# Performance work log

Measured on AMD Instinct MI355X. Metric: run time of the kernel, lower is better.

The kernel has to match this reference:

```python
import jax, jax.numpy as jnp
import numpy as np

N = 4096       # nodes
NFEAT = 256    # feature dim
NCLASS = 16
E = 65536      # edges = N * avg_degree(16)
NLAYER = 4
ALPHA = 0.5    # blancealpha (non-trainable)
LAMBDA_1 = 1.0
LAMBDA_2 = 1.0
EPS = 1e-12    # F.normalize eps


def setup_inputs() -> dict:
    key = jax.random.key(0)
    ks = jax.random.split(key, 9)
    feat = jax.random.normal(ks[0], (N, NFEAT), dtype=jnp.float32)
    z0 = jax.random.uniform(ks[1], (N, NFEAT), dtype=jnp.float32)       # torch.rand init of z
    w1 = jax.random.uniform(ks[2], (N, N), dtype=jnp.float32)           # uniform_(0,1)
    EA = jax.random.uniform(ks[3], (N, N), dtype=jnp.float32)           # uniform_(0,1)
    w2_w = jax.random.normal(ks[4], (2 * NFEAT, NCLASS), dtype=jnp.float32) * 0.05
    w2_b = jnp.zeros((NCLASS,), dtype=jnp.float32)
    edge_i = jax.random.randint(ks[5], (E,), 0, N, dtype=jnp.int32)
    edge_j = jax.random.randint(ks[6], (E,), 0, N, dtype=jnp.int32)
    edge_val = jax.random.uniform(ks[7], (E,), dtype=jnp.float32)
    # dense adjacency from the sparse edge list (coalesce -> duplicate indices sum)
    adj = jnp.zeros((N, N), dtype=jnp.float32).at[edge_i, edge_j].add(edge_val)
    # w22 = ones with zeros at edge positions (as in __init__)
    w22 = jnp.ones((N, N), dtype=jnp.float32).at[edge_i, edge_j].set(0.0)
    return dict(feat=feat, z0=z0, w1=w1, EA=EA, w2_w=w2_w, w2_b=w2_b,
                adj=adj, w22=w22, edge_val=edge_val, edge_i=edge_i, edge_j=edge_j)


def reference(feat, z0, w1, EA, w2_w, w2_b, adj, w22, edge_val, edge_i, edge_j):
    n = feat.shape[0]
    y = feat                      # y starts as feat
    z = z0                        # torch.rand init, passed in for determinism
    EP = jnp.ones((n, n), dtype=feat.dtype)
    masked_EA = ALPHA * EA * w22  # constant across layers
    for _ in range(NLAYER):
        # dropout is identity in eval mode (training=False)
        A = adj * EP + masked_EA            # [n, n]
        yyT = y @ y.T                       # [n, n] (reused; same values as the two torch.mm calls)
        temp = EP.T @ y + A @ y - yyT @ y   # [n, nfeat]
        temp = jax.nn.sigmoid(w1 @ temp)
        y_n = (LAMBDA_2 / 2) * temp + feat
        z_n = z - A @ z                     # (I - A) @ z
        # ans(z, adj): edgewise ||z_i - z_j|| * adj_val scattered to dense
        P = jnp.linalg.norm(z[edge_i] - z[edge_j], axis=1) * edge_val   # [E]
        M = jnp.zeros((n, n), dtype=z.dtype).at[edge_i, edge_j].add(P)
        EP = (LAMBDA_2 * (yyT - masked_EA) - LAMBDA_1 * 0.5 * M) / LAMBDA_2
        y, z = y_n, z_n
    # F.normalize(p=2, dim=1)
    y = y / jnp.maximum(jnp.linalg.norm(y, axis=1, keepdims=True), EPS)
    z = z / jnp.maximum(jnp.linalg.norm(z, axis=1, keepdims=True), EPS)
    p = jnp.concatenate([z, y], axis=1)     # [n, 2*nfeat]
    logits = p @ w2_w + w2_b
    return jax.nn.log_softmax(logits, axis=1)
```

## Files before the change

### kernel.cpp

```cpp
#include <hip/hip_runtime.h>

#define Nn 4096
#define Ff 256
#define NCLS 16
#define Ne 65536
#define TSZ 262144
#define NF (Nn*Ff)
#define NNx (Nn*Nn)
#define KS 8

typedef unsigned short u16;
typedef unsigned int u32;
typedef __attribute__((ext_vector_type(8))) short short8;
typedef __attribute__((ext_vector_type(4))) float float4v;

__device__ __forceinline__ float bfh(u16 u){ return __uint_as_float(((u32)u)<<16); }
__device__ __forceinline__ u16 f2bf(float f){
    u32 u = __float_as_uint(f);
    return (u16)((u + 0x7FFFu + ((u>>16)&1u)) >> 16);
}
__device__ __forceinline__ void gload16(const u16* g, u16* l){
    __builtin_amdgcn_global_load_lds(
        (const __attribute__((address_space(1))) u32*)(const void*)g,
        (__attribute__((address_space(3))) u32*)(void*)l, 16, 0, 0);
}

__device__ float g_yA[NF], g_yB[NF], g_zA[NF], g_zB[NF], g_t1[NF], g_T1[NF];
__device__ float g_Gp[16*Ff*Ff], g_col[Ff], g_P[Ne], g_cc[Ne], g_hV[TSZ];
__device__ float g_pb[(size_t)3*KS*NF];
__device__ u32 g_hK[TSZ], g_slot[Ne];
__device__ int g_cntI[Nn], g_cntJ[Nn], g_rpI[Nn+1], g_rpJ[Nn+1], g_fI[Nn], g_fJ[Nn];
__device__ int g_lI[Ne], g_lJ[Ne];
__device__ __align__(16) u16 g_w1h[NNx], g_w1l[NNx];
__device__ __align__(16) u16 g_meh[NNx], g_mel[NNx];
__device__ __align__(16) u16 g_mth[NNx], g_mtl[NNx];
__device__ __align__(16) u16 g_x0h[NF], g_x0l[NF], g_x1h[NF], g_x1l[NF];
__device__ __align__(16) u16 g_zt0h[NF], g_zt0l[NF], g_zt1h[NF], g_zt1l[NF];
__device__ __align__(16) u16 g_yr0h[NF], g_yr0l[NF], g_yr1h[NF], g_yr1l[NF];
__device__ __align__(16) u16 g_tth[NF], g_ttl[NF];
__device__ __align__(16) u16 g_gth[Ff*Ff], g_gtl[Ff*Ff];

__global__ __launch_bounds__(256) void k_zero(float* p, int n){
    int i = blockIdx.x*256 + threadIdx.x;
    if (i < n) p[i] = 0.f;
}
__global__ __launch_bounds__(256) void k_zeroi(int* p, int n){
    int i = blockIdx.x*256 + threadIdx.x;
    if (i < n) p[i] = 0;
}
__global__ __launch_bounds__(256) void k_fillc(float* p, float v, int n){
    int i = blockIdx.x*256 + threadIdx.x;
    if (i < n) p[i] = v;
}
__global__ __launch_bounds__(256) void k_hkeys_clear(u32* K){
    int i = blockIdx.x*256 + threadIdx.x;
    if (i < TSZ) K[i] = 0xFFFFFFFFu;
}
__global__ __launch_bounds__(256) void k_hsetup(u32* K, u32* slot, const int* ei, const int* ej){
    int e = blockIdx.x*256 + threadIdx.x;
    if (e >= Ne) return;
    u32 key = ((u32)ei[e] << 12) | (u32)ej[e];
    u32 h = (key * 2654435761u) & (TSZ-1);
    for (;;){
        u32 old = atomicCAS(&K[h], 0xFFFFFFFFu, key);
        if (old == 0xFFFFFFFFu || old == key){ slot[e] = h; break; }
        h = (h+1) & (TSZ-1);
    }
}

__global__ __launch_bounds__(256) void k_count(int* cntI, int* cntJ, const int* ei, const int* ej){
    int e = blockIdx.x*256 + threadIdx.x;
    if (e < Ne){ atomicAdd(&cntI[ei[e]], 1); atomicAdd(&cntJ[ej[e]], 1); }
}
// ... 48 lines not shown
    __syncthreads();
    for (int q = 0; q < 16; ++q){
        int r = q*4 + rr;
        float v = T[c][r];
        size_t o = (size_t)(c0+r)*Nn + r0 + c;
        u16 h = f2bf(v); mth[o] = h; mtl[o] = f2bf(v - bfh(h));
    }
}
__global__ __launch_bounds__(256) void k_splitXT(u16* hi, u16* lo, const float* X){
    __shared__ float T[64][65];
    int r0 = blockIdx.y*64, c0 = blockIdx.x*64;
    int c = threadIdx.x & 63, rr = threadIdx.x >> 6;
    for (int q = 0; q < 16; ++q){
        int r = q*4 + rr;
        T[r][c] = X[(size_t)(r0+r)*Ff + c0 + c];
    }
    __syncthreads();
    for (int q = 0; q < 16; ++q){
        int r = q*4 + rr;
        float v = T[c][r];
        size_t o = (size_t)(c0+r)*Nn + r0 + c;
        u16 h = f2bf(v); hi[o] = h; lo[o] = f2bf(v - bfh(h));
    }
}
__global__ __launch_bounds__(256) void k_splitGT(u16* hi, u16* lo, const float* Gp){
    __shared__ float T[64][65];
    int r0 = blockIdx.y*64, c0 = blockIdx.x*64;
    int c = threadIdx.x & 63, rr = threadIdx.x >> 6;
    for (int q = 0; q < 16; ++q){
        int r = q*4 + rr;
        float v = 0.f;
        #pragma unroll
        for (int z = 0; z < 16; ++z) v += Gp[z*(Ff*Ff) + (r0+r)*Ff + c0 + c];
        T[r][c] = v;
    }
    __syncthreads();
    for (int q = 0; q < 16; ++q){
        int r = q*4 + rr;
        float v = T[c][r];
        int o = (c0+r)*Ff + r0 + c;
        u16 h = f2bf(v); hi[o] = h; lo[o] = f2bf(v - bfh(h));
    }
}

__device__ __forceinline__ void mm_tile(
    const u16* __restrict__ Ahp, const u16* __restrict__ Alp,
    const u16* __restrict__ Bhp, const u16* __restrict__ Blp,
    size_t sA, size_t sB, int i0, int j0, int k0,
    u16* LAh, u16* LAl, u16* LBh, u16* LBl,
    float4v* acc, int lane, int w)
{
    const int g1 = w*64 + lane;
    const int g2 = g1 + 256;
    const int r1 = g1>>3, p1 = g1&7, r2 = g2>>3, p2 = g2&7;
    const size_t a1 = (size_t)(i0+r1)*sA + (size_t)(k0 + ((p1 ^ (r1&7))<<3));
    const size_t a2 = (size_t)(i0+r2)*sA + (size_t)(k0 + ((p2 ^ (r2&7))<<3));
    const size_t b1 = (size_t)(j0+r1)*sB + (size_t)(k0 + ((p1 ^ (r1&7))<<3));
    const size_t b2 = (size_t)(j0+r2)*sB + (size_t)(k0 + ((p2 ^ (r2&7))<<3));
    __syncthreads();
    gload16(Ahp + a1, LAh + g1*8);
    gload16(Ahp + a2, LAh + g2*8);
    gload16(Alp + a1, LAl + g1*8);
    gload16(Alp + a2, LAl + g2*8);
    gload16(Bhp + b1, LBh + g1*8);
    gload16(Bhp + b2, LBh + g2*8);
    gload16(Blp + b1, LBl + g1*8);
// ... 38 lines not shown
        for (int r = 0; r < 4; ++r){
            int grow = i0 + w*16 + (lane>>4)*4 + r;
            int gcol = j0 + c*16 + (lane&15);
            size_t idx = (size_t)grow*Ff + gcol;
            float v = acc[c][r];
            if constexpr (V == 3) out[idx] = aux1[idx] - v;
            if constexpr (V == 4) out[idx] = aux1[gcol] - v;
            if constexpr (V == 5) out[idx] = v;
        }
}

__global__ __launch_bounds__(256) void k_gram_mm(float* __restrict__ Gp,
        const u16* __restrict__ Ahp, const u16* __restrict__ Alp,
        const u16* __restrict__ Bhp, const u16* __restrict__ Blp){
    __shared__ u16 LAh[4096], LAl[4096], LBh[4096], LBl[4096];
    const int tid = threadIdx.x, lane = tid & 63, w = tid >> 6;
    const int j0 = blockIdx.x*64, i0 = blockIdx.y*64, kb = blockIdx.z*256;
    float4v acc[4];
    #pragma unroll
    for (int c = 0; c < 4; ++c) acc[c] = (float4v){0.f,0.f,0.f,0.f};
    for (int kt = 0; kt < 4; ++kt)
        mm_tile(Ahp, Alp, Bhp, Blp, (size_t)Nn, (size_t)Nn, i0, j0, kb + kt*64, LAh, LAl, LBh, LBl, acc, lane, w);
    float* op = Gp + (size_t)blockIdx.z*(Ff*Ff);
    #pragma unroll
    for (int c = 0; c < 4; ++c)
        #pragma unroll
        for (int r = 0; r < 4; ++r){
            int grow = i0 + w*16 + (lane>>4)*4 + r;
            int gcol = j0 + c*16 + (lane&15);
            op[grow*Ff + gcol] = acc[c][r];
        }
}

__global__ __launch_bounds__(512) void k_mmB(float* __restrict__ pb,
        const u16* __restrict__ A0h, const u16* __restrict__ A0l,
        const u16* __restrict__ B0h, const u16* __restrict__ B0l,
        const u16* __restrict__ A1h, const u16* __restrict__ A1l,
        const u16* __restrict__ B1h, const u16* __restrict__ B1l,
        const u16* __restrict__ A2h, const u16* __restrict__ A2l,
        const u16* __restrict__ B2h, const u16* __restrict__ B2l){
    __shared__ u16 LAh[4096], LAl[4096], LBh[16384], LBl[16384];
    const int tid = threadIdx.x, lane = tid & 63, w = tid >> 6;
    const int z = blockIdx.x, i0 = blockIdx.y*64, bat = blockIdx.z;
    const u16 *Ah, *Al, *Bh, *Bl;
    if (bat == 0){ Ah = A0h; Al = A0l; Bh = B0h; Bl = B0l; }
    else if (bat == 1){ Ah = A1h; Al = A1l; Bh = B1h; Bl = B1l; }
    else { Ah = A2h; Al = A2l; Bh = B2h; Bl = B2l; }
    const int wr = w >> 2, wc = w & 3;
    float4v acc[2][4];
    #pragma unroll
    for (int m = 0; m < 2; ++m)
        #pragma unroll
        for (int n = 0; n < 4; ++n) acc[m][n] = (float4v){0.f,0.f,0.f,0.f};

    const int ra = tid >> 3, pa = tid & 7;
    const size_t aoff = (size_t)(i0+ra)*Nn + (size_t)((pa ^ (ra&7))<<3);

    for (int kt = 0; kt < 8; ++kt){
        const int k0 = z*512 + kt*64;
        __syncthreads();
        gload16(Ah + aoff + k0, LAh + tid*8);
        gload16(Al + aoff + k0, LAl + tid*8);
        #pragma unroll
        for (int it = 0; it < 4; ++it){
            int g = it*512 + tid;
            int r = g >> 3, p = g & 7;
            size_t b = (size_t)r*Nn + (size_t)(k0 + ((p ^ (r&7))<<3));
            gload16(Bh + b, LBh + g*8);
            gload16(Bl + b, LBl + g*8);
        }
        __syncthreads();
        #pragma unroll
        for (int kk = 0; kk < 2; ++kk){
            const int ch = kk*4 + (lane>>4);
            short8 ah0, ah1, al0, al1;
            {
                const int arow = wr*32 + (lane&15);
                const int ao = arow*64 + ((ch ^ (arow&7))<<3);
                ah0 = *(const short8*)(LAh + ao);
                al0 = *(const short8*)(LAl + ao);
            }
            {
                const int arow = wr*32 + 16 + (lane&15);
                const int ao = arow*64 + ((ch ^ (arow&7))<<3);
                ah1 = *(const short8*)(LAh + ao);
                al1 = *(const short8*)(LAl + ao);
            }
            #pragma unroll
            for (int n = 0; n < 4; ++n){
                const int bcol = wc*64 + n*16 + (lane&15);
                const int bo = bcol*64 + ((ch ^ (bcol&7))<<3);
                short8 bh = *(const short8*)(LBh + bo);
                short8 bl = *(const short8*)(LBl + bo);
                acc[0][n] = __builtin_amdgcn_mfma_f32_16x16x32_bf16(ah0, bh, acc[0][n], 0,0,0);
                acc[0][n] = __builtin_amdgcn_mfma_f32_16x16x32_bf16(ah0, bl, acc[0][n], 0,0,0);
                acc[0][n] = __builtin_amdgcn_mfma_f32_16x16x32_bf16(al0, bh, acc[0][n], 0,0,0);
                acc[1][n] = __builtin_amdgcn_mfma_f32_16x16x32_bf16(ah1, bh, acc[1][n], 0,0,0);
                acc[1][n] = __builtin_amdgcn_mfma_f32_16x16x32_bf16(ah1, bl, acc[1][n], 0,0,0);
                acc[1][n] = __builtin_amdgcn_mfma_f32_16x16x32_bf16(al1, bh, acc[1][n], 0,0,0);
            }
        }
    }
    float* op = pb + ((size_t)bat*KS + z)*NF;
    #pragma unroll
    for (int m = 0; m < 2; ++m)
        #pragma unroll
        for (int n = 0; n < 4; ++n)
            #pragma unroll
            for (int r = 0; r < 4; ++r){
                int row = i0 + wr*32 + m*16 + (lane>>4)*4 + r;
                int col = wc*64 + n*16 + (lane&15);
                op[(size_t)row*Ff + col] = acc[m][n][r];
            }
}

template<int HASM, int DOSPLIT>
__global__ __launch_bounds__(256) void k_redT1(float* __restrict__ t1, const float* __restrict__ pb,
        u16* __restrict__ th, u16* __restrict__ tl){
    __shared__ float T[64][65];
    const int c0 = blockIdx.x*64, r0 = blockIdx.y*64;
    const int c = threadIdx.x & 63, rr = threadIdx.x >> 6;
    for (int q = 0; q < 16; ++q){
        int row = q*4 + rr;
        size_t idx = (size_t)(r0+row)*Ff + c0 + c;
        float s = 0.f;
        #pragma unroll
        for (int p = 0; p < KS; ++p) s += pb[(size_t)p*NF + idx];
        if constexpr (HASM){
            #pragma unroll
            for (int p = 0; p < KS; ++p) s -= pb[((size_t)2*KS + p)*NF + idx];
        }
        float val = t1[idx] + s;
        t1[idx] = val;
        if constexpr (DOSPLIT) T[row][c] = val;
    }
    if constexpr (DOSPLIT){
        __syncthreads();
        for (int q = 0; q < 16; ++q){
            int r = q*4 + rr;
            float v = T[c][r];
            size_t o = (size_t)(c0+r)*Nn + r0 + c;
            u16 h = f2bf(v); th[o] = h; tl[o] = f2bf(v - bfh(h));
        }
    }
}

__global__ __launch_bounds__(256) void k_redY(float* __restrict__ yn, const float* __restrict__ pb,
        const float* __restrict__ feat, u16* __restrict__ rh, u16* __restrict__ rl,
        u16* __restrict__ th, u16* __restrict__ tl){
    __shared__ float T[64][65];
    const int c0 = blockIdx.x*64, r0 = blockIdx.y*64;
    const int c = threadIdx.x & 63, rr = threadIdx.x >> 6;
    for (int q = 0; q < 16; ++q){
        int row = q*4 + rr;
        size_t idx = (size_t)(r0+row)*Ff + c0 + c;
        float s = 0.f;
        #pragma unroll
        for (int p = 0; p < KS; ++p) s += pb[(size_t)p*NF + idx];
        float val = feat[idx] + 0.5f*(1.f/(1.f+expf(-s)));
        yn[idx] = val;
        u16 h = f2bf(val); rh[idx] = h; rl[idx] = f2bf(val - bfh(h));
        T[row][c] = val;
    }
    __syncthreads();
    for (int q = 0; q < 16; ++q){
        int r = q*4 + rr;
        float v = T[c][r];
        size_t o = (size_t)(c0+r)*Nn + r0 + c;
        u16 h = f2bf(v); th[o] = h; tl[o] = f2bf(v - bfh(h));
    }
}

__global__ __launch_bounds__(256) void k_csrTZ(float* __restrict__ t1, float* __restrict__ zn,
        const float* __restrict__ y, const float* __restrict__ z, const float* __restrict__ pb1,
        const float* __restrict__ cc, const float* __restrict__ P,
        const int* __restrict__ rpI, const int* __restrict__ lI, const int* __restrict__ ej,
        const int* __restrict__ rpJ, const int* __restrict__ lJ, const int* __restrict__ ei,
        int useM){
    const int r = blockIdx.x, f = threadIdx.x;
    float at = 0.f, az = 0.f;
    const int b0 = rpI[r], b1 = rpI[r+1];
    for (int p = b0; p < b1; ++p){
        int e = lI[p];
        float ce = cc[e];
        int j = ej[e];
        at += ce * y[(size_t)j*Ff + f];
        az += ce * z[(size_t)j*Ff + f];
    }
    if (useM){
        const int c0 = rpJ[r], c1 = rpJ[r+1];
        for (int p = c0; p < c1; ++p){
            int e = lJ[p];
            at -= 0.5f * P[e] * y[(size_t)ei[e]*Ff + f];
        }
    }
    size_t idx = (size_t)r*Ff + f;
    float dz = 0.f;
    #pragma unroll
    for (int p = 0; p < KS; ++p) dz += pb1[(size_t)p*NF + idx];
    t1[idx] += at;
    zn[idx] = z[idx] - dz - az;
}

__global__ __launch_bounds__(256) void k_colsum(float* col, const float* __restrict__ y){
    int j = threadIdx.x;
    int r0 = blockIdx.x*64;
    float s = 0.f;
    for (int i = 0; i < 64; ++i) s += y[(size_t)(r0+i)*Ff + j];
    atomicAdd(&col[j], s);
}

__global__ __launch_bounds__(256) void k_pacc(float* __restrict__ P, float* __restrict__ hV,
        const float* __restrict__ z, const int* __restrict__ ei, const int* __restrict__ ej,
        const float* __restrict__ ev, const u32* __restrict__ slot){
    int e = blockIdx.x*4 + (threadIdx.x >> 6);
    int lane = threadIdx.x & 63;
    int i = ei[e], j = ej[e];
    float s = 0.f;
    #pragma unroll
    for (int q = 0; q < 4; ++q){
        int f = lane + q*64;
        float d = z[(size_t)i*Ff + f] - z[(size_t)j*Ff + f];
        s += d*d;
    }
    #pragma unroll
    for (int o = 32; o; o >>= 1) s += __shfl_xor(s, o);
    if (lane == 0){
        float v = sqrtf(s) * ev[e];
        P[e] = v;
        atomicAdd(&hV[slot[e]], v);
    }
}
// ... 60 lines not shown
        for (int cc = 0; cc < NCLS; ++cc) se += expf(lg[cc]-m);
        ml[0] = m; ml[1] = logf(se);
    }
    __syncthreads();
    if (t < NCLS) out[(size_t)node*NCLS + t] = lg[t] - ml[0] - ml[1];
}

extern "C" void kernel_launch(void* const* d_in, const int* in_sizes, int n_in,
                              void* d_out, int out_size, void* d_ws, size_t ws_size,
                              hipStream_t stream){
    const float* feat = (const float*)d_in[0];
    const float* z0i  = (const float*)d_in[1];
    const float* w1p  = (const float*)d_in[2];
    const float* EAp  = (const float*)d_in[3];
    const float* w2w  = (const float*)d_in[4];
    const float* w2b  = (const float*)d_in[5];
    const float* w22p = (const float*)d_in[7];
    const float* evp  = (const float*)d_in[8];
    const int* ei   = (const int*)d_in[9];
    const int* ej   = (const int*)d_in[10];
    float* out = (float*)d_out;

    int ok = (n_in == 11) && (out_size == Nn*NCLS)
           && in_sizes[0]==NF && in_sizes[1]==NF && in_sizes[2]==NNx && in_sizes[3]==NNx
           && in_sizes[4]==2*Ff*NCLS && in_sizes[5]==NCLS && in_sizes[6]==NNx && in_sizes[7]==NNx
           && in_sizes[8]==Ne && in_sizes[9]==Ne && in_sizes[10]==Ne;
    if (!ok){
        k_fillc<<<(out_size+255)/256, 256, 0, stream>>>(out, -100.0f, out_size);
        return;
    }

    float *yA,*yB,*zA,*zB,*t1,*T1,*Gp,*col,*P,*cc,*hV,*pb; u32 *hK,*slot;
    int *cntI,*cntJ,*rpI,*rpJ,*fI,*fJ,*lI,*lJ;
    u16 *w1h,*w1l,*meh,*mel,*mth,*mtl,*gth,*gtl,*tth,*ttl;
    u16 *xh[2],*xl[2],*zth[2],*ztl[2],*yrh[2],*yrl[2];
    hipGetSymbolAddress((void**)&yA,  HIP_SYMBOL(g_yA));
    hipGetSymbolAddress((void**)&yB,  HIP_SYMBOL(g_yB));
    hipGetSymbolAddress((void**)&zA,  HIP_SYMBOL(g_zA));
    hipGetSymbolAddress((void**)&zB,  HIP_SYMBOL(g_zB));
    hipGetSymbolAddress((void**)&t1,  HIP_SYMBOL(g_t1));
    hipGetSymbolAddress((void**)&T1,  HIP_SYMBOL(g_T1));
    hipGetSymbolAddress((void**)&Gp,  HIP_SYMBOL(g_Gp));
    hipGetSymbolAddress((void**)&col, HIP_SYMBOL(g_col));
    hipGetSymbolAddress((void**)&P,   HIP_SYMBOL(g_P));
    hipGetSymbolAddress((void**)&cc,  HIP_SYMBOL(g_cc));
    hipGetSymbolAddress((void**)&hV,  HIP_SYMBOL(g_hV));
    hipGetSymbolAddress((void**)&pb,  HIP_SYMBOL(g_pb));
    hipGetSymbolAddress((void**)&hK,  HIP_SYMBOL(g_hK));
    hipGetSymbolAddress((void**)&slot,HIP_SYMBOL(g_slot));
    hipGetSymbolAddress((void**)&cntI,HIP_SYMBOL(g_cntI));
    hipGetSymbolAddress((void**)&cntJ,HIP_SYMBOL(g_cntJ));
    hipGetSymbolAddress((void**)&rpI, HIP_SYMBOL(g_rpI));
    hipGetSymbolAddress((void**)&rpJ, HIP_SYMBOL(g_rpJ));
    hipGetSymbolAddress((void**)&fI,  HIP_SYMBOL(g_fI));
    hipGetSymbolAddress((void**)&fJ,  HIP_SYMBOL(g_fJ));
    hipGetSymbolAddress((void**)&lI,  HIP_SYMBOL(g_lI));
    hipGetSymbolAddress((void**)&lJ,  HIP_SYMBOL(g_lJ));
    hipGetSymbolAddress((void**)&w1h, HIP_SYMBOL(g_w1h));
    hipGetSymbolAddress((void**)&w1l, HIP_SYMBOL(g_w1l));
    hipGetSymbolAddress((void**)&meh, HIP_SYMBOL(g_meh));
    hipGetSymbolAddress((void**)&mel, HIP_SYMBOL(g_mel));
    hipGetSymbolAddress((void**)&mth, HIP_SYMBOL(g_mth));
    hipGetSymbolAddress((void**)&mtl, HIP_SYMBOL(g_mtl));
    hipGetSymbolAddress((void**)&gth, HIP_SYMBOL(g_gth));
    hipGetSymbolAddress((void**)&gtl, HIP_SYMBOL(g_gtl));
    hipGetSymbolAddress((void**)&tth, HIP_SYMBOL(g_tth));
    hipGetSymbolAddress((void**)&ttl, HIP_SYMBOL(g_ttl));
    hipGetSymbolAddress((void**)&xh[0], HIP_SYMBOL(g_x0h));
    hipGetSymbolAddress((void**)&xl[0], HIP_SYMBOL(g_x0l));
    hipGetSymbolAddress((void**)&xh[1], HIP_SYMBOL(g_x1h));
    hipGetSymbolAddress((void**)&xl[1], HIP_SYMBOL(g_x1l));
    hipGetSymbolAddress((void**)&zth[0], HIP_SYMBOL(g_zt0h));
    hipGetSymbolAddress((void**)&ztl[0], HIP_SYMBOL(g_zt0l));
    hipGetSymbolAddress((void**)&zth[1], HIP_SYMBOL(g_zt1h));
    hipGetSymbolAddress((void**)&ztl[1], HIP_SYMBOL(g_zt1l));
    hipGetSymbolAddress((void**)&yrh[0], HIP_SYMBOL(g_yr0h));
    hipGetSymbolAddress((void**)&yrl[0], HIP_SYMBOL(g_yr0l));
    hipGetSymbolAddress((void**)&yrh[1], HIP_SYMBOL(g_yr1h));
    hipGetSymbolAddress((void**)&yrl[1], HIP_SYMBOL(g_yr1l));

    const dim3 gSmall(Ff/64, Nn/64);
    const dim3 gXT(Ff/64, Nn/64);
    const dim3 gME(Nn/64, Nn/64);
    const dim3 gGT(Ff/64, Ff/64);
    const dim3 gGram(4, 4, 16);
    const dim3 gRed(Ff/64, Nn/64);

    k_split4<<<NNx/4/256, 256, 0, stream>>>((ushort4*)w1h, (ushort4*)w1l, (const float4*)w1p, NNx/4);
    k_splitME2<<<gME, 256, 0, stream>>>(meh, mel, mth, mtl, EAp, w22p);
    k_split4<<<NF/4/256, 256, 0, stream>>>((ushort4*)yrh[0], (ushort4*)yrl[0], (const float4*)feat, NF/4);
    k_splitXT<<<gXT, 256, 0, stream>>>(xh[0], xl[0], feat);
    k_splitXT<<<gXT, 256, 0, stream>>>(zth[0], ztl[0], z0i);
    k_hkeys_clear<<<TSZ/256, 256, 0, stream>>>(hK);
    k_hsetup<<<Ne/256, 256, 0, stream>>>(hK, slot, ei, ej);
    k_zeroi<<<Nn/256, 256, 0, stream>>>(cntI, Nn);
    k_zeroi<<<Nn/256, 256, 0, stream>>>(cntJ, Nn);
    k_count<<<Ne/256, 256, 0, stream>>>(cntI, cntJ, ei, ej);
    k_scan<<<1, 1024, 0, stream>>>(cntI, rpI);
    k_scan<<<1, 1024, 0, stream>>>(cntJ, rpJ);
    k_zeroi<<<Nn/256, 256, 0, stream>>>(fI, Nn);
    k_zeroi<<<Nn/256, 256, 0, stream>>>(fJ, Nn);
    k_fillcsr<<<Ne/256, 256, 0, stream>>>(rpI, rpJ, fI, fJ, lI, lJ, ei, ej);

    const float* yv = feat;  const float* zv = z0i;
    for (int t = 1; t <= 4; ++t){
        int ri = (t-1) & 1, wi = t & 1;
        u16 *xhc = xh[ri], *xlc = xl[ri], *xhn = xh[wi], *xln = xl[wi];
        u16 *zthc = zth[ri], *ztlc = ztl[ri], *zthn = zth[wi], *ztln = ztl[wi];
        u16 *yrhc = yrh[ri], *yrlc = yrl[ri], *yrhn = yrh[wi], *yrln = yrl[wi];
        float* yn = (t & 1) ? yA : yB;
        float* zn = (t & 1) ? zA : zB;
        const float* ccv = (t == 1) ? evp : cc;

        k_gram_mm<<<gGram, 256, 0, stream>>>(Gp, xhc, xlc, xhc, xlc);
        k_splitGT<<<gGT, 256, 0, stream>>>(gth, gtl, Gp);
        if (t == 1){
            k_zero<<<1, 256, 0, stream>>>(col, Ff);
            k_colsum<<<64, 256, 0, stream>>>(col, yv);
            k_mm<4><<<gSmall, 256, 0, stream>>>(t1, yrhc, yrlc, gth, gtl, col);
        } else {
            k_mm<3><<<gSmall, 256, 0, stream>>>(t1, yrhc, yrlc, gth, gtl, T1);
        }
        {
            int nb = (t == 1) ? 2 : 3;
            dim3 gB(KS, Nn/64, nb);
            k_mmB<<<gB, 512, 0, stream>>>(pb,
                meh, mel, xhc, xlc,
                meh, mel, zthc, ztlc,
                mth, mtl, xhc, xlc);
        }
        k_csrTZ<<<Nn, 256, 0, stream>>>(t1, zn, yv, zv, pb + (size_t)KS*NF, ccv, P,
                                        rpI, lI, ej, rpJ, lJ, ei, (t >= 2) ? 1 : 0);
        if (t == 1) k_redT1<0,1><<<gRed, 256, 0, stream>>>(t1, pb, tth, ttl);
        else        k_redT1<1,1><<<gRed, 256, 0, stream>>>(t1, pb, tth, ttl);
        if (t < 4)
            k_splitXT<<<gXT, 256, 0, stream>>>(zthn, ztln, zn);
        {
            dim3 gB(KS, Nn/64, 1);
            k_mmB<<<gB, 512, 0, stream>>>(pb,
                w1h, w1l, tth, ttl,
                w1h, w1l, tth, ttl,
                w1h, w1l, tth, ttl);
        }
        k_redY<<<gRed, 256, 0, stream>>>(yn, pb, feat, yrhn, yrln, xhn, xln);
        if (t < 4){
            k_zero<<<TSZ/256, 256, 0, stream>>>(hV, TSZ);
            k_pacc<<<Ne/4, 256, 0, stream>>>(P, hV, zv, ei, ej, evp, slot);
            k_ep<<<Ne/4, 256, 0, stream>>>(cc, yv, ei, ej, evp, hV, slot);
            k_gram_mm<<<gGram, 256, 0, stream>>>(Gp, xhc, xlc, xhn, xln);
            k_splitGT<<<gGT, 256, 0, stream>>>(gth, gtl, Gp);
            k_mm<5><<<gSmall, 256, 0, stream>>>(T1, yrhc, yrlc, gth, gtl, nullptr);
        }
        yv = yn; zv = zn;
    }
    k_head<<<Nn, 256, 0, stream>>>(out, yv, zv, w2w, w2b);
}
```

Baseline: 1.479 ms.

## Double-buffer LDS in split-bf16 GEMM and retile to 128x128 blocks

The split-K bf16x3 GEMM kernel now stages the next 64-wide K slice into a second LDS buffer while computing on the current one, replacing the load-sync-compute-sync pattern. The block tile changes from 64 rows by all 256 columns to 128x128, with wave layout 4x2, and the grid is reshaped so blockIdx.x encodes column half and K split. The aim is to hide global-to-LDS latency and balance A and B tile loads. In exchange, LDS use per block doubles to 128KB, which limits occupancy. There is also no wait on the async global_load_lds before the barrier, so it relies on the barrier's implicit vmcnt behaviour.

Result: slower. 1.546 ms (+4.5%).

```diff
diff --git a/kernel.cpp b/kernel.cpp
--- a/kernel.cpp
+++ b/kernel.cpp
@@ -264,69 +264,74 @@
         const u16* __restrict__ B1h, const u16* __restrict__ B1l,
         const u16* __restrict__ A2h, const u16* __restrict__ A2l,
         const u16* __restrict__ B2h, const u16* __restrict__ B2l){
-    __shared__ u16 LAh[4096], LAl[4096], LBh[16384], LBl[16384];
+    __shared__ u16 LA[2][2][8192];
+    __shared__ u16 LB[2][2][8192];
     const int tid = threadIdx.x, lane = tid & 63, w = tid >> 6;
-    const int z = blockIdx.x, i0 = blockIdx.y*64, bat = blockIdx.z;
+    const int jb = blockIdx.x & 1, kp = blockIdx.x >> 1;
+    const int j0 = jb*128, i0 = blockIdx.y*128, bat = blockIdx.z;
+    const int kbase = kp*512;
     const u16 *Ah, *Al, *Bh, *Bl;
     if (bat == 0){ Ah = A0h; Al = A0l; Bh = B0h; Bl = B0l; }
     else if (bat == 1){ Ah = A1h; Al = A1l; Bh = B1h; Bl = B1l; }
     else { Ah = A2h; Al = A2l; Bh = B2h; Bl = B2l; }
-    const int wr = w >> 2, wc = w & 3;
+    const int wr = w >> 1, wc = w & 1;
     float4v acc[2][4];
     #pragma unroll
     for (int m = 0; m < 2; ++m)
         #pragma unroll
         for (int n = 0; n < 4; ++n) acc[m][n] = (float4v){0.f,0.f,0.f,0.f};
 
-    const int ra = tid >> 3, pa = tid & 7;
-    const size_t aoff = (size_t)(i0+ra)*Nn + (size_t)((pa ^ (ra&7))<<3);
-
+    const int srow = tid >> 3, sp = tid & 7;
+    const size_t aoff0 = (size_t)(i0 + srow)*Nn + (size_t)((sp ^ (srow&7))<<3);
+    const size_t aoff1 = aoff0 + (size_t)64*Nn;
+    const size_t boff0 = (size_t)(j0 + srow)*Nn + (size_t)((sp ^ (srow&7))<<3);
+    const size_t boff1 = boff0 + (size_t)64*Nn;
+    const int d0 = tid*8, d1 = tid*8 + 4096;
+
+#define STAGE(B, K0) { \
+    gload16(Ah + aoff0 + (K0), &LA[B][0][d0]); \
+    gload16(Ah + aoff1 + (K0), &LA[B][0][d1]); \
+    gload16(Al + aoff0 + (K0), &LA[B][1][d0]); \
+    gload16(Al + aoff1 + (K0), &LA[B][1][d1]); \
+    gload16(Bh + boff0 + (K0), &LB[B][0][d0]); \
+    gload16(Bh + boff1 + (K0), &LB[B][0][d1]); \
+    gload16(Bl + boff0 + (K0), &LB[B][1][d0]); \
+    gload16(Bl + boff1 + (K0), &LB[B][1][d1]); }
+
+#define COMPUTE(B) { \
+    _Pragma("unroll") \
+    for (int kk = 0; kk < 2; ++kk){ \
+        const int ch = kk*4 + (lane>>4); \
+        short8 ah0, al0, ah1, al1; \
+        { int ar = wr*32 + (lane&15); int ao = ar*64 + ((ch ^ (ar&7))<<3); \
+          ah0 = *(const short8*)&LA[B][0][ao]; al0 = *(const short8*)&LA[B][1][ao]; } \
+        { int ar = wr*32 + 16 + (lane&15); int ao = ar*64 + ((ch ^ (ar&7))<<3); \
+          ah1 = *(const short8*)&LA[B][0][ao]; al1 = *(const short8*)&LA[B][1][ao]; } \
+        _Pragma("unroll") \
+        for (int n = 0; n < 4; ++n){ \
+            int bc = wc*64 + n*16 + (lane&15); int bo = bc*64 + ((ch ^ (bc&7))<<3); \
+            short8 bh = *(const short8*)&LB[B][0][bo]; \
+            short8 bl = *(const short8*)&LB[B][1][bo]; \
+            acc[0][n] = __builtin_amdgcn_mfma_f32_16x16x32_bf16(ah0, bh, acc[0][n], 0,0,0); \
+            acc[0][n] = __builtin_amdgcn_mfma_f32_16x16x32_bf16(ah0, bl, acc[0][n], 0,0,0); \
+            acc[0][n] = __builtin_amdgcn_mfma_f32_16x16x32_bf16(al0, bh, acc[0][n], 0,0,0); \
+            acc[1][n] = __builtin_amdgcn_mfma_f32_16x16x32_bf16(ah1, bh, acc[1][n], 0,0,0); \
+            acc[1][n] = __builtin_amdgcn_mfma_f32_16x16x32_bf16(ah1, bl, acc[1][n], 0,0,0); \
+            acc[1][n] = __builtin_amdgcn_mfma_f32_16x16x32_bf16(al1, bh, acc[1][n], 0,0,0); \
+        } \
+    } }
+
+    STAGE(0, kbase)
+    __syncthreads();
     for (int kt = 0; kt < 8; ++kt){
-        const int k0 = z*512 + kt*64;
+        if (kt < 7) STAGE((kt+1)&1, kbase + (kt+1)*64)
+        COMPUTE(kt&1)
         __syncthreads();
-        gload16(Ah + aoff + k0, LAh + tid*8);
-        gload16(Al + aoff + k0, LAl + tid*8);
-        #pragma unroll
-        for (int it = 0; it < 4; ++it){
-            int g = it*512 + tid;
-            int r = g >> 3, p = g & 7;
-            size_t b = (size_t)r*Nn + (size_t)(k0 + ((p ^ (r&7))<<3));
-            gload16(Bh + b, LBh + g*8);
-            gload16(Bl + b, LBl + g*8);
-        }
-        __syncthreads();
-        #pragma unroll
-        for (int kk = 0; kk < 2; ++kk){
-            const int ch = kk*4 + (lane>>4);
-            short8 ah0, ah1, al0, al1;
-            {
-                const int arow = wr*32 + (lane&15);
-                const int ao = arow*64 + ((ch ^ (arow&7))<<3);
-                ah0 = *(const short8*)(LAh + ao);
-                al0 = *(const short8*)(LAl + ao);
-            }
-            {
-                const int arow = wr*32 + 16 + (lane&15);
-                const int ao = arow*64 + ((ch ^ (arow&7))<<3);
-                ah1 = *(const short8*)(LAh + ao);
-                al1 = *(const short8*)(LAl + ao);
-            }
-            #pragma unroll
-            for (int n = 0; n < 4; ++n){
-                const int bcol = wc*64 + n*16 + (lane&15);
-                const int bo = bcol*64 + ((ch ^ (bcol&7))<<3);
-                short8 bh = *(const short8*)(LBh + bo);
-                short8 bl = *(const short8*)(LBl + bo);
-                acc[0][n] = __builtin_amdgcn_mfma_f32_16x16x32_bf16(ah0, bh, acc[0][n], 0,0,0);
-                acc[0][n] = __builtin_amdgcn_mfma_f32_16x16x32_bf16(ah0, bl, acc[0][n], 0,0,0);
-                acc[0][n] = __builtin_amdgcn_mfma_f32_16x16x32_bf16(al0, bh, acc[0][n], 0,0,0);
-                acc[1][n] = __builtin_amdgcn_mfma_f32_16x16x32_bf16(ah1, bh, acc[1][n], 0,0,0);
-                acc[1][n] = __builtin_amdgcn_mfma_f32_16x16x32_bf16(ah1, bl, acc[1][n], 0,0,0);
-                acc[1][n] = __builtin_amdgcn_mfma_f32_16x16x32_bf16(al1, bh, acc[1][n], 0,0,0);
-            }
-        }
-    }
-    float* op = pb + ((size_t)bat*KS + z)*NF;
+    }
+#undef STAGE
+#undef COMPUTE
+
+    float* op = pb + ((size_t)bat*KS + kp)*NF;
     #pragma unroll
     for (int m = 0; m < 2; ++m)
         #pragma unroll
@@ -334,7 +339,7 @@
             #pragma unroll
             for (int r = 0; r < 4; ++r){
                 int row = i0 + wr*32 + m*16 + (lane>>4)*4 + r;
-                int col = wc*64 + n*16 + (lane&15);
+                int col = j0 + wc*64 + n*16 + (lane&15);
                 op[(size_t)row*Ff + col] = acc[m][n][r];
             }
 }
@@ -640,7 +645,7 @@
         }
         {
             int nb = (t == 1) ? 2 : 3;
-            dim3 gB(KS, Nn/64, nb);
+            dim3 gB(16, Nn/128, nb);
             k_mmB<<<gB, 512, 0, stream>>>(pb,
                 meh, mel, xhc, xlc,
                 meh, mel, zthc, ztlc,
@@ -653,7 +658,7 @@
         if (t < 4)
             k_splitXT<<<gXT, 256, 0, stream>>>(zthn, ztln, zn);
         {
-            dim3 gB(KS, Nn/64, 1);
+            dim3 gB(16, Nn/128, 1);
             k_mmB<<<gB, 512, 0, stream>>>(pb,
                 w1h, w1l, tth, ttl,
                 w1h, w1l, tth, ttl,
```

## Fuse consecutive Gram products and retile the big split-K GEMM to 256-thread blocks

Applied to the files above, without the earlier changes.

The next layer's Gram matrix x_n^T x_n is now computed in the same launch as the cross Gram x_c^T x_n, with results written to a second split buffer. This removes the separate Gram and split launches at the start of layers 2-4. The main split-K GEMM kernel changes from 512-thread blocks covering all 256 output columns to 256-thread blocks covering 128 columns each. Each wave now computes one 16-row strip across eight column tiles, and the grid doubles. This roughly halves LDS per block, which may raise occupancy, but each A tile is now loaded twice across column blocks.

After: 1.458 ms. Within noise of the previous version (-1.4%).

```diff
diff --git a/kernel.cpp b/kernel.cpp
--- a/kernel.cpp
+++ b/kernel.cpp
@@ -26,7 +26,7 @@
 }
 
 __device__ float g_yA[NF], g_yB[NF], g_zA[NF], g_zB[NF], g_t1[NF], g_T1[NF];
-__device__ float g_Gp[16*Ff*Ff], g_col[Ff], g_P[Ne], g_cc[Ne], g_hV[TSZ];
+__device__ float g_Gp[32*Ff*Ff], g_col[Ff], g_P[Ne], g_cc[Ne], g_hV[TSZ];
 __device__ float g_pb[(size_t)3*KS*NF];
 __device__ u32 g_hK[TSZ], g_slot[Ne];
 __device__ int g_cntI[Nn], g_cntJ[Nn], g_rpI[Nn+1], g_rpJ[Nn+1], g_fI[Nn], g_fJ[Nn];
@@ -39,6 +39,7 @@
 __device__ __align__(16) u16 g_yr0h[NF], g_yr0l[NF], g_yr1h[NF], g_yr1l[NF];
 __device__ __align__(16) u16 g_tth[NF], g_ttl[NF];
 __device__ __align__(16) u16 g_gth[Ff*Ff], g_gtl[Ff*Ff];
+__device__ __align__(16) u16 g_g2h[Ff*Ff], g_g2l[Ff*Ff];
 
 __global__ __launch_bounds__(256) void k_zero(float* p, int n){
     int i = blockIdx.x*256 + threadIdx.x;
@@ -153,6 +154,30 @@
         float v = 0.f;
         #pragma unroll
         for (int z = 0; z < 16; ++z) v += Gp[z*(Ff*Ff) + (r0+r)*Ff + c0 + c];
+        T[r][c] = v;
+    }
+    __syncthreads();
+    for (int q = 0; q < 16; ++q){
+        int r = q*4 + rr;
+        float v = T[c][r];
+        int o = (c0+r)*Ff + r0 + c;
+        u16 h = f2bf(v); hi[o] = h; lo[o] = f2bf(v - bfh(h));
+    }
+}
+__global__ __launch_bounds__(256) void k_splitGT2(u16* h0, u16* l0, u16* h1, u16* l1,
+                                                  const float* Gp){
+    __shared__ float T[64][65];
+    const int which = blockIdx.z;
+    u16* hi = which ? h1 : h0;
+    u16* lo = which ? l1 : l0;
+    const float* G = Gp + (size_t)which*16*(Ff*Ff);
+    int r0 = blockIdx.y*64, c0 = blockIdx.x*64;
+    int c = threadIdx.x & 63, rr = threadIdx.x >> 6;
+    for (int q = 0; q < 16; ++q){
+        int r = q*4 + rr;
+        float v = 0.f;
+        #pragma unroll
+        for (int z = 0; z < 16; ++z) v += G[z*(Ff*Ff) + (r0+r)*Ff + c0 + c];
         T[r][c] = v;
     }
     __syncthreads();
@@ -257,86 +282,100 @@
         }
 }
 
-__global__ __launch_bounds__(512) void k_mmB(float* __restrict__ pb,
+__global__ __launch_bounds__(256) void k_gram_mm2(float* __restrict__ Gp,
+        const u16* __restrict__ Ahp, const u16* __restrict__ Alp,
+        const u16* __restrict__ Bhp, const u16* __restrict__ Blp){
+    __shared__ u16 LAh[4096], LAl[4096], LBh[4096], LBl[4096];
+    const int tid = threadIdx.x, lane = tid & 63, w = tid >> 6;
+    const int j0 = blockIdx.x*64, i0 = blockIdx.y*64;
+    const int pz = blockIdx.z;
+    const int kb = (pz & 15)*256, which = pz >> 4;
+    const u16* pAh = which ? Bhp : Ahp;
+    const u16* pAl = which ? Blp : Alp;
+    float4v acc[4];
+    #pragma unroll
+    for (int c = 0; c < 4; ++c) acc[c] = (float4v){0.f,0.f,0.f,0.f};
+    for (int kt = 0; kt < 4; ++kt)
+        mm_tile(pAh, pAl, Bhp, Blp, (size_t)Nn, (size_t)Nn, i0, j0, kb + kt*64, LAh, LAl, LBh, LBl, acc, lane, w);
+    float* op = Gp + (size_t)pz*(Ff*Ff);
+    #pragma unroll
+    for (int c = 0; c < 4; ++c)
+        #pragma unroll
+        for (int r = 0; r < 4; ++r){
+            int grow = i0 + w*16 + (lane>>4)*4 + r;
+            int gcol = j0 + c*16 + (lane&15);
+            op[grow*Ff + gcol] = acc[c][r];
+        }
+}
+
+__global__ __launch_bounds__(256) void k_mmB(float* __restrict__ pb,
         const u16* __restrict__ A0h, const u16* __restrict__ A0l,
         const u16* __restrict__ B0h, const u16* __restrict__ B0l,
         const u16* __restrict__ A1h, const u16* __restrict__ A1l,
         const u16* __restrict__ B1h, const u16* __restrict__ B1l,
         const u16* __restrict__ A2h, const u16* __restrict__ A2l,
         const u16* __restrict__ B2h, const u16* __restrict__ B2l){
-    __shared__ u16 LAh[4096], LAl[4096], LBh[16384], LBl[16384];
+    __shared__ u16 LAh[4096], LAl[4096], LBh[8192], LBl[8192];
     const int tid = threadIdx.x, lane = tid & 63, w = tid >> 6;
-    const int z = blockIdx.x, i0 = blockIdx.y*64, bat = blockIdx.z;
+    const int jb = blockIdx.x & 1, kp = blockIdx.x >> 1;
+    const int j0 = jb*128, i0 = blockIdx.y*64, bat = blockIdx.z;
     const u16 *Ah, *Al, *Bh, *Bl;
     if (bat == 0){ Ah = A0h; Al = A0l; Bh = B0h; Bl = B0l; }
     else if (bat == 1){ Ah = A1h; Al = A1l; Bh = B1h; Bl = B1l; }
     else { Ah = A2h; Al = A2l; Bh = B2h; Bl = B2l; }
-    const int wr = w >> 2, wc = w & 3;
-    float4v acc[2][4];
-    #pragma unroll
-    for (int m = 0; m < 2; ++m)
-        #pragma unroll
-        for (int n = 0; n < 4; ++n) acc[m][n] = (float4v){0.f,0.f,0.f,0.f};
-
-    const int ra = tid >> 3, pa = tid & 7;
-    const size_t aoff = (size_t)(i0+ra)*Nn + (size_t)((pa ^ (ra&7))<<3);
+    float4v acc[8];
+    #pragma unroll
+    for (int n = 0; n < 8; ++n) acc[n] = (float4v){0.f,0.f,0.f,0.f};
+
+    const int r1 = tid >> 3, p1 = tid & 7;
+    const int g2 = tid + 256, r2 = g2 >> 3, p2 = g2 & 7;
+    const size_t aoff1 = (size_t)(i0+r1)*Nn + (size_t)((p1 ^ (r1&7))<<3);
+    const size_t aoff2 = (size_t)(i0+r2)*Nn + (size_t)((p2 ^ (r2&7))<<3);
 
     for (int kt = 0; kt < 8; ++kt){
-        const int k0 = z*512 + kt*64;
+        const int k0 = kp*512 + kt*64;
         __syncthreads();
-        gload16(Ah + aoff + k0, LAh + tid*8);
-        gload16(Al + aoff + k0, LAl + tid*8);
+        gload16(Ah + aoff1 + k0, LAh + tid*8);
+        gload16(Ah + aoff2 + k0, LAh + g2*8);
+        gload16(Al + aoff1 + k0, LAl + tid*8);
+        gload16(Al + aoff2 + k0, LAl + g2*8);
         #pragma unroll
         for (int it = 0; it < 4; ++it){
-            int g = it*512 + tid;
+            int g = it*256 + tid;
             int r = g >> 3, p = g & 7;
-            size_t b = (size_t)r*Nn + (size_t)(k0 + ((p ^ (r&7))<<3));
+            size_t b = (size_t)(j0+r)*Nn + (size_t)(k0 + ((p ^ (r&7))<<3));
             gload16(Bh + b, LBh + g*8);
             gload16(Bl + b, LBl + g*8);
         }
         __syncthreads();
+        const int arow = w*16 + (lane&15);
         #pragma unroll
         for (int kk = 0; kk < 2; ++kk){
             const int ch = kk*4 + (lane>>4);
-            short8 ah0, ah1, al0, al1;
-            {
-                const int arow = wr*32 + (lane&15);
-                const int ao = arow*64 + ((ch ^ (arow&7))<<3);
-                ah0 = *(const short8*)(LAh + ao);
-                al0 = *(const short8*)(LAl + ao);
-            }
-            {
-                const int arow = wr*32 + 16 + (lane&15);
-                const int ao = arow*64 + ((ch ^ (arow&7))<<3);
-                ah1 = *(const short8*)(LAh + ao);
-                al1 = *(const short8*)(LAl + ao);
-            }
+            const int ao = arow*64 + ((ch ^ (arow&7))<<3);
+            short8 ah = *(const short8*)(LAh + ao);
+            short8 al = *(const short8*)(LAl + ao);
             #pragma unroll
-            for (int n = 0; n < 4; ++n){
-                const int bcol = wc*64 + n*16 + (lane&15);
-                const int bo = bcol*64 + ((ch ^ (bcol&7))<<3);
+            for (int n = 0; n < 8; ++n){
+                const int bc = n*16 + (lane&15);
+                const int bo = bc*64 + ((ch ^ (bc&7))<<3);
                 short8 bh = *(const short8*)(LBh + bo);
                 short8 bl = *(const short8*)(LBl + bo);
-                acc[0][n] = __builtin_amdgcn_mfma_f32_16x16x32_bf16(ah0, bh, acc[0][n], 0,0,0);
-                acc[0][n] = __builtin_amdgcn_mfma_f32_16x16x32_bf16(ah0, bl, acc[0][n], 0,0,0);
-                acc[0][n] = __builtin_amdgcn_mfma_f32_16x16x32_bf16(al0, bh, acc[0][n], 0,0,0);
-                acc[1][n] = __builtin_amdgcn_mfma_f32_16x16x32_bf16(ah1, bh, acc[1][n], 0,0,0);
-                acc[1][n] = __builtin_amdgcn_mfma_f32_16x16x32_bf16(ah1, bl, acc[1][n], 0,0,0);
-                acc[1][n] = __builtin_amdgcn_mfma_f32_16x16x32_bf16(al1, bh, acc[1][n], 0,0,0);
+                acc[n] = __builtin_amdgcn_mfma_f32_16x16x32_bf16(ah, bh, acc[n], 0,0,0);
+                acc[n] = __builtin_amdgcn_mfma_f32_16x16x32_bf16(ah, bl, acc[n], 0,0,0);
+                acc[n] = __builtin_amdgcn_mfma_f32_16x16x32_bf16(al, bh, acc[n], 0,0,0);
             }
         }
     }
-    float* op = pb + ((size_t)bat*KS + z)*NF;
-    #pragma unroll
-    for (int m = 0; m < 2; ++m)
-        #pragma unroll
-        for (int n = 0; n < 4; ++n)
-            #pragma unroll
-            for (int r = 0; r < 4; ++r){
-                int row = i0 + wr*32 + m*16 + (lane>>4)*4 + r;
-                int col = wc*64 + n*16 + (lane&15);
-                op[(size_t)row*Ff + col] = acc[m][n][r];
-            }
+    float* op = pb + ((size_t)bat*KS + kp)*NF;
+    #pragma unroll
+    for (int n = 0; n < 8; ++n)
+        #pragma unroll
+        for (int r = 0; r < 4; ++r){
+            int row = i0 + w*16 + (lane>>4)*4 + r;
+            int col = j0 + n*16 + (lane&15);
+            op[(size_t)row*Ff + col] = acc[n][r];
+        }
 }
 
 template<int HASM, int DOSPLIT>
@@ -549,7 +588,7 @@
 
     float *yA,*yB,*zA,*zB,*t1,*T1,*Gp,*col,*P,*cc,*hV,*pb; u32 *hK,*slot;
     int *cntI,*cntJ,*rpI,*rpJ,*fI,*fJ,*lI,*lJ;
-    u16 *w1h,*w1l,*meh,*mel,*mth,*mtl,*gth,*gtl,*tth,*ttl;
+    u16 *w1h,*w1l,*meh,*mel,*mth,*mtl,*gth,*gtl,*g2h,*g2l,*tth,*ttl;
     u16 *xh[2],*xl[2],*zth[2],*ztl[2],*yrh[2],*yrl[2];
     hipGetSymbolAddress((void**)&yA,  HIP_SYMBOL(g_yA));
     hipGetSymbolAddress((void**)&yB,  HIP_SYMBOL(g_yB));
@@ -581,6 +620,8 @@
     hipGetSymbolAddress((void**)&mtl, HIP_SYMBOL(g_mtl));
     hipGetSymbolAddress((void**)&gth, HIP_SYMBOL(g_gth));
     hipGetSymbolAddress((void**)&gtl, HIP_SYMBOL(g_gtl));
+    hipGetSymbolAddress((void**)&g2h, HIP_SYMBOL(g_g2h));
+    hipGetSymbolAddress((void**)&g2l, HIP_SYMBOL(g_g2l));
     hipGetSymbolAddress((void**)&tth, HIP_SYMBOL(g_tth));
     hipGetSymbolAddress((void**)&ttl, HIP_SYMBOL(g_ttl));
     hipGetSymbolAddress((void**)&xh[0], HIP_SYMBOL(g_x0h));
@@ -601,6 +642,8 @@
     const dim3 gME(Nn/64, Nn/64);
     const dim3 gGT(Ff/64, Ff/64);
     const dim3 gGram(4, 4, 16);
+    const dim3 gGram2(4, 4, 32);
+    const dim3 gGT2(4, 4, 2);
     const dim3 gRed(Ff/64, Nn/64);
 
     k_split4<<<NNx/4/256, 256, 0, stream>>>((ushort4*)w1h, (ushort4*)w1l, (const float4*)w1p, NNx/4);
@@ -629,19 +672,19 @@
         float* zn = (t & 1) ? zA : zB;
         const float* ccv = (t == 1) ? evp : cc;
 
-        k_gram_mm<<<gGram, 256, 0, stream>>>(Gp, xhc, xlc, xhc, xlc);
-        k_splitGT<<<gGT, 256, 0, stream>>>(gth, gtl, Gp);
         if (t == 1){
+            k_gram_mm<<<gGram, 256, 0, stream>>>(Gp, xhc, xlc, xhc, xlc);
+            k_splitGT<<<gGT, 256, 0, stream>>>(gth, gtl, Gp);
             k_zero<<<1, 256, 0, stream>>>(col, Ff);
             k_colsum<<<64, 256, 0, stream>>>(col, yv);
             k_mm<4><<<gSmall, 256, 0, stream>>>(t1, yrhc, yrlc, gth, gtl, col);
         } else {
-            k_mm<3><<<gSmall, 256, 0, stream>>>(t1, yrhc, yrlc, gth, gtl, T1);
+            k_mm<3><<<gSmall, 256, 0, stream>>>(t1, yrhc, yrlc, g2h, g2l, T1);
         }
         {
             int nb = (t == 1) ? 2 : 3;
-            dim3 gB(KS, Nn/64, nb);
-            k_mmB<<<gB, 512, 0, stream>>>(pb,
+            dim3 gB(16, Nn/64, nb);
+            k_mmB<<<gB, 256, 0, stream>>>(pb,
                 meh, mel, xhc, xlc,
                 meh, mel, zthc, ztlc,
                 mth, mtl, xhc, xlc);
@@ -653,8 +696,8 @@
         if (t < 4)
             k_splitXT<<<gXT, 256, 0, stream>>>(zthn, ztln, zn);
         {
-            dim3 gB(KS, Nn/64, 1);
-            k_mmB<<<gB, 512, 0, stream>>>(pb,
+            dim3 gB(16, Nn/64, 1);
+            k_mmB<<<gB, 256, 0, stream>>>(pb,
                 w1h, w1l, tth, ttl,
                 w1h, w1l, tth, ttl,
                 w1h, w1l, tth, ttl);
@@ -664,8 +707,8 @@
             k_zero<<<TSZ/256, 256, 0, stream>>>(hV, TSZ);
             k_pacc<<<Ne/4, 256, 0, stream>>>(P, hV, zv, ei, ej, evp, slot);
             k_ep<<<Ne/4, 256, 0, stream>>>(cc, yv, ei, ej, evp, hV, slot);
-            k_gram_mm<<<gGram, 256, 0, stream>>>(Gp, xhc, xlc, xhn, xln);
-            k_splitGT<<<gGT, 256, 0, stream>>>(gth, gtl, Gp);
+            k_gram_mm2<<<gGram2, 256, 0, stream>>>(Gp, xhc, xlc, xhn, xln);
+            k_splitGT2<<<gGT2, 256, 0, stream>>>(gth, gtl, g2h, g2l, Gp);
             k_mm<5><<<gSmall, 256, 0, stream>>>(T1, yrhc, yrlc, gth, gtl, nullptr);
         }
         yv = yn; zv = zn;
```

## Batch next-layer Gram with cross Gram and retune mmB split-K per call

Applied to the files above, without the earlier changes.

The Gram X_n^T X_n for the next layer is now computed in the same launch as the cross Gram X_c^T X_n, using a doubled z grid and a two-way split/transpose kernel. This removes one Gram and one split kernel launch per layer and gives more parallel blocks. The split-K factor of the batched mmB is also made a template parameter: 4 for the adjacency products and 8 for the w1 product. That cuts partial-buffer traffic and reduction work for the first, at the cost of fewer blocks in that launch.

Result: faster. 1.352 ms (median of 2 runs) (-8.5%).

```diff
diff --git a/kernel.cpp b/kernel.cpp
--- a/kernel.cpp
+++ b/kernel.cpp
@@ -7,7 +7,6 @@
 #define TSZ 262144
 #define NF (Nn*Ff)
 #define NNx (Nn*Nn)
-#define KS 8
 
 typedef unsigned short u16;
 typedef unsigned int u32;
@@ -26,8 +25,8 @@
 }
 
 __device__ float g_yA[NF], g_yB[NF], g_zA[NF], g_zB[NF], g_t1[NF], g_T1[NF];
-__device__ float g_Gp[16*Ff*Ff], g_col[Ff], g_P[Ne], g_cc[Ne], g_hV[TSZ];
-__device__ float g_pb[(size_t)3*KS*NF];
+__device__ float g_Gp[32*Ff*Ff], g_col[Ff], g_P[Ne], g_cc[Ne], g_hV[TSZ];
+__device__ float g_pb[(size_t)24*NF];
 __device__ u32 g_hK[TSZ], g_slot[Ne];
 __device__ int g_cntI[Nn], g_cntJ[Nn], g_rpI[Nn+1], g_rpJ[Nn+1], g_fI[Nn], g_fJ[Nn];
 __device__ int g_lI[Ne], g_lJ[Ne];
@@ -39,6 +38,7 @@
 __device__ __align__(16) u16 g_yr0h[NF], g_yr0l[NF], g_yr1h[NF], g_yr1l[NF];
 __device__ __align__(16) u16 g_tth[NF], g_ttl[NF];
 __device__ __align__(16) u16 g_gth[Ff*Ff], g_gtl[Ff*Ff];
+__device__ __align__(16) u16 g_g2h[Ff*Ff], g_g2l[Ff*Ff];
 
 __global__ __launch_bounds__(256) void k_zero(float* p, int n){
     int i = blockIdx.x*256 + threadIdx.x;
@@ -153,6 +153,30 @@
         float v = 0.f;
         #pragma unroll
         for (int z = 0; z < 16; ++z) v += Gp[z*(Ff*Ff) + (r0+r)*Ff + c0 + c];
+        T[r][c] = v;
+    }
+    __syncthreads();
+    for (int q = 0; q < 16; ++q){
+        int r = q*4 + rr;
+        float v = T[c][r];
+        int o = (c0+r)*Ff + r0 + c;
+        u16 h = f2bf(v); hi[o] = h; lo[o] = f2bf(v - bfh(h));
+    }
+}
+__global__ __launch_bounds__(256) void k_splitGT2(u16* h0, u16* l0, u16* h1, u16* l1,
+                                                  const float* Gp){
+    __shared__ float T[64][65];
+    const int which = blockIdx.z;
+    u16* hi = which ? h1 : h0;
+    u16* lo = which ? l1 : l0;
+    const float* G = Gp + (size_t)which*16*(Ff*Ff);
+    int r0 = blockIdx.y*64, c0 = blockIdx.x*64;
+    int c = threadIdx.x & 63, rr = threadIdx.x >> 6;
+    for (int q = 0; q < 16; ++q){
+        int r = q*4 + rr;
+        float v = 0.f;
+        #pragma unroll
+        for (int z = 0; z < 16; ++z) v += G[z*(Ff*Ff) + (r0+r)*Ff + c0 + c];
         T[r][c] = v;
     }
     __syncthreads();
@@ -257,6 +281,33 @@
         }
 }
 
+__global__ __launch_bounds__(256) void k_gram_mm2(float* __restrict__ Gp,
+        const u16* __restrict__ Ahp, const u16* __restrict__ Alp,
+        const u16* __restrict__ Bhp, const u16* __restrict__ Blp){
+    __shared__ u16 LAh[4096], LAl[4096], LBh[4096], LBl[4096];
+    const int tid = threadIdx.x, lane = tid & 63, w = tid >> 6;
+    const int j0 = blockIdx.x*64, i0 = blockIdx.y*64;
+    const int pz = blockIdx.z;
+    const int kb = (pz & 15)*256, which = pz >> 4;
+    const u16* pAh = which ? Bhp : Ahp;
+    const u16* pAl = which ? Blp : Alp;
+    float4v acc[4];
+    #pragma unroll
+    for (int c = 0; c < 4; ++c) acc[c] = (float4v){0.f,0.f,0.f,0.f};
+    for (int kt = 0; kt < 4; ++kt)
+        mm_tile(pAh, pAl, Bhp, Blp, (size_t)Nn, (size_t)Nn, i0, j0, kb + kt*64, LAh, LAl, LBh, LBl, acc, lane, w);
+    float* op = Gp + (size_t)pz*(Ff*Ff);
+    #pragma unroll
+    for (int c = 0; c < 4; ++c)
+        #pragma unroll
+        for (int r = 0; r < 4; ++r){
+            int grow = i0 + w*16 + (lane>>4)*4 + r;
+            int gcol = j0 + c*16 + (lane&15);
+            op[grow*Ff + gcol] = acc[c][r];
+        }
+}
+
+template<int KSP>
 __global__ __launch_bounds__(512) void k_mmB(float* __restrict__ pb,
         const u16* __restrict__ A0h, const u16* __restrict__ A0l,
         const u16* __restrict__ B0h, const u16* __restrict__ B0l,
@@ -280,9 +331,10 @@
 
     const int ra = tid >> 3, pa = tid & 7;
     const size_t aoff = (size_t)(i0+ra)*Nn + (size_t)((pa ^ (ra&7))<<3);
-
-    for (int kt = 0; kt < 8; ++kt){
-        const int k0 = z*512 + kt*64;
+    constexpr int NKT = 64 / KSP;
+
+    for (int kt = 0; kt < NKT; ++kt){
+        const int k0 = z*(NKT*64) + kt*64;
         __syncthreads();
         gload16(Ah + aoff + k0, LAh + tid*8);
         gload16(Al + aoff + k0, LAl + tid*8);
@@ -326,7 +378,7 @@
             }
         }
     }
-    float* op = pb + ((size_t)bat*KS + z)*NF;
+    float* op = pb + ((size_t)bat*KSP + z)*NF;
     #pragma unroll
     for (int m = 0; m < 2; ++m)
         #pragma unroll
@@ -350,10 +402,10 @@
         size_t idx = (size_t)(r0+row)*Ff + c0 + c;
         float s = 0.f;
         #pragma unroll
-        for (int p = 0; p < KS; ++p) s += pb[(size_t)p*NF + idx];
+        for (int p = 0; p < 4; ++p) s += pb[(size_t)p*NF + idx];
         if constexpr (HASM){
             #pragma unroll
-            for (int p = 0; p < KS; ++p) s -= pb[((size_t)2*KS + p)*NF + idx];
+            for (int p = 0; p < 4; ++p) s -= pb[((size_t)8 + p)*NF + idx];
         }
         float val = t1[idx] + s;
         t1[idx] = val;
@@ -381,7 +433,7 @@
         size_t idx = (size_t)(r0+row)*Ff + c0 + c;
         float s = 0.f;
         #pragma unroll
-        for (int p = 0; p < KS; ++p) s += pb[(size_t)p*NF + idx];
+        for (int p = 0; p < 8; ++p) s += pb[(size_t)p*NF + idx];
         float val = feat[idx] + 0.5f*(1.f/(1.f+expf(-s)));
         yn[idx] = val;
         u16 h = f2bf(val); rh[idx] = h; rl[idx] = f2bf(val - bfh(h));
@@ -422,7 +474,7 @@
     size_t idx = (size_t)r*Ff + f;
     float dz = 0.f;
     #pragma unroll
-    for (int p = 0; p < KS; ++p) dz += pb1[(size_t)p*NF + idx];
+    for (int p = 0; p < 4; ++p) dz += pb1[(size_t)p*NF + idx];
     t1[idx] += at;
     zn[idx] = z[idx] - dz - az;
 }
@@ -549,7 +601,7 @@
 
     float *yA,*yB,*zA,*zB,*t1,*T1,*Gp,*col,*P,*cc,*hV,*pb; u32 *hK,*slot;
     int *cntI,*cntJ,*rpI,*rpJ,*fI,*fJ,*lI,*lJ;
-    u16 *w1h,*w1l,*meh,*mel,*mth,*mtl,*gth,*gtl,*tth,*ttl;
+    u16 *w1h,*w1l,*meh,*mel,*mth,*mtl,*gth,*gtl,*g2h,*g2l,*tth,*ttl;
     u16 *xh[2],*xl[2],*zth[2],*ztl[2],*yrh[2],*yrl[2];
     hipGetSymbolAddress((void**)&yA,  HIP_SYMBOL(g_yA));
     hipGetSymbolAddress((void**)&yB,  HIP_SYMBOL(g_yB));
@@ -581,6 +633,8 @@
     hipGetSymbolAddress((void**)&mtl, HIP_SYMBOL(g_mtl));
     hipGetSymbolAddress((void**)&gth, HIP_SYMBOL(g_gth));
     hipGetSymbolAddress((void**)&gtl, HIP_SYMBOL(g_gtl));
+    hipGetSymbolAddress((void**)&g2h, HIP_SYMBOL(g_g2h));
+    hipGetSymbolAddress((void**)&g2l, HIP_SYMBOL(g_g2l));
     hipGetSymbolAddress((void**)&tth, HIP_SYMBOL(g_tth));
     hipGetSymbolAddress((void**)&ttl, HIP_SYMBOL(g_ttl));
     hipGetSymbolAddress((void**)&xh[0], HIP_SYMBOL(g_x0h));
@@ -601,6 +655,8 @@
     const dim3 gME(Nn/64, Nn/64);
     const dim3 gGT(Ff/64, Ff/64);
     const dim3 gGram(4, 4, 16);
+    const dim3 gGram2(4, 4, 32);
+    const dim3 gGT2(4, 4, 2);
     const dim3 gRed(Ff/64, Nn/64);
 
     k_split4<<<NNx/4/256, 256, 0, stream>>>((ushort4*)w1h, (ushort4*)w1l, (const float4*)w1p, NNx/4);
@@ -629,32 +685,32 @@
         float* zn = (t & 1) ? zA : zB;
         const float* ccv = (t == 1) ? evp : cc;
 
-        k_gram_mm<<<gGram, 256, 0, stream>>>(Gp, xhc, xlc, xhc, xlc);
-        k_splitGT<<<gGT, 256, 0, stream>>>(gth, gtl, Gp);
         if (t == 1){
+            k_gram_mm<<<gGram, 256, 0, stream>>>(Gp, xhc, xlc, xhc, xlc);
+            k_splitGT<<<gGT, 256, 0, stream>>>(gth, gtl, Gp);
             k_zero<<<1, 256, 0, stream>>>(col, Ff);
             k_colsum<<<64, 256, 0, stream>>>(col, yv);
             k_mm<4><<<gSmall, 256, 0, stream>>>(t1, yrhc, yrlc, gth, gtl, col);
         } else {
-            k_mm<3><<<gSmall, 256, 0, stream>>>(t1, yrhc, yrlc, gth, gtl, T1);
+            k_mm<3><<<gSmall, 256, 0, stream>>>(t1, yrhc, yrlc, g2h, g2l, T1);
         }
         {
             int nb = (t == 1) ? 2 : 3;
-            dim3 gB(KS, Nn/64, nb);
-            k_mmB<<<gB, 512, 0, stream>>>(pb,
+            dim3 gB(4, Nn/64, nb);
+            k_mmB<4><<<gB, 512, 0, stream>>>(pb,
                 meh, mel, xhc, xlc,
                 meh, mel, zthc, ztlc,
                 mth, mtl, xhc, xlc);
         }
-        k_csrTZ<<<Nn, 256, 0, stream>>>(t1, zn, yv, zv, pb + (size_t)KS*NF, ccv, P,
+        k_csrTZ<<<Nn, 256, 0, stream>>>(t1, zn, yv, zv, pb + (size_t)4*NF, ccv, P,
                                         rpI, lI, ej, rpJ, lJ, ei, (t >= 2) ? 1 : 0);
         if (t == 1) k_redT1<0,1><<<gRed, 256, 0, stream>>>(t1, pb, tth, ttl);
         else        k_redT1<1,1><<<gRed, 256, 0, stream>>>(t1, pb, tth, ttl);
         if (t < 4)
             k_splitXT<<<gXT, 256, 0, stream>>>(zthn, ztln, zn);
         {
-            dim3 gB(KS, Nn/64, 1);
-            k_mmB<<<gB, 512, 0, stream>>>(pb,
+            dim3 gB(8, Nn/64, 1);
+            k_mmB<8><<<gB, 512, 0, stream>>>(pb,
                 w1h, w1l, tth, ttl,
                 w1h, w1l, tth, ttl,
                 w1h, w1l, tth, ttl);
@@ -664,8 +720,8 @@
             k_zero<<<TSZ/256, 256, 0, stream>>>(hV, TSZ);
             k_pacc<<<Ne/4, 256, 0, stream>>>(P, hV, zv, ei, ej, evp, slot);
             k_ep<<<Ne/4, 256, 0, stream>>>(cc, yv, ei, ej, evp, hV, slot);
-            k_gram_mm<<<gGram, 256, 0, stream>>>(Gp, xhc, xlc, xhn, xln);
-            k_splitGT<<<gGT, 256, 0, stream>>>(gth, gtl, Gp);
+            k_gram_mm2<<<gGram2, 256, 0, stream>>>(Gp, xhc, xlc, xhn, xln);
+            k_splitGT2<<<gGT2, 256, 0, stream>>>(gth, gtl, g2h, g2l, Gp);
             k_mm<5><<<gSmall, 256, 0, stream>>>(T1, yrhc, yrlc, gth, gtl, nullptr);
         }
         yv = yn; zv = zn;
```
